# Optimization experiments

Measured on AMD Instinct MI355X. Metric: run time of the kernel, lower is better.

The kernel has to match this reference:

```python
import jax, jax.numpy as jnp
import numpy as np

N_ATOMS = 10000
N_HIDDEN = 75


def setup_inputs() -> dict:
    key = jax.random.key(0)
    k1, k2, k3, k4 = jax.random.split(key, 4)
    n_edges, n_pair_features = 64000, 14
    pair_features = jax.random.normal(k1, (n_edges, n_pair_features), dtype=jnp.float32)
    atom_features = jax.random.normal(k2, (N_ATOMS, N_HIDDEN), dtype=jnp.float32)
    atom_to_pair = jnp.sort(
        jax.random.randint(k3, (n_edges, 2), 0, N_ATOMS), axis=0
    ).astype(jnp.int64)
    # glorot_uniform for W [n_pair_features, n_hidden*n_hidden]
    fan_in, fan_out = n_pair_features, N_HIDDEN * N_HIDDEN
    limit = np.sqrt(6.0 / (fan_in + fan_out)).astype(np.float32)
    W = jax.random.uniform(k4, (fan_in, fan_out), minval=-limit, maxval=limit, dtype=jnp.float32)
    b = jnp.zeros((fan_out,), dtype=jnp.float32)
    return {"pair_features": pair_features, "atom_features": atom_features,
            "atom_to_pair": atom_to_pair, "W": W, "b": b}


def reference(pair_features, atom_features, atom_to_pair, W, b):
    # A: per-edge [n_hidden, n_hidden] matrices from pair features
    A = (pair_features @ W + b).reshape(-1, N_HIDDEN, N_HIDDEN)  # [E, H, H]
    # gather destination-atom features, batched matvec
    l = atom_features[atom_to_pair[:, 1]]                         # [E, H]
    out = jnp.einsum('ehk,ek->eh', A, l)                          # [E, H]
    # scatter-reduce to source atoms
    return jax.ops.segment_sum(out, atom_to_pair[:, 0], num_segments=N_ATOMS)
```

## Files before the change

kernel.cpp:

```cpp
#include <hip/hip_runtime.h>
#include <hip/hip_bf16.h>
#include <stdint.h>

constexpr int NA   = 10000;
constexpr int NH   = 75;
constexpr int NPF  = 14;
constexpr int NW   = 5625;
constexpr int NCOL = 1200;
constexpr int KP   = 104;
constexpr int MROW = 10112;
constexpr int WROW = 1208;
constexpr int JSL  = 38;

typedef __attribute__((ext_vector_type(8))) __bf16 bf16x8;
typedef __attribute__((ext_vector_type(4))) float floatx4;

__device__ __forceinline__ uint32_t f2bf_bits(float f) {
    uint32_t u = __float_as_uint(f);
    return (u + 0x7fffu + ((u >> 16) & 1u)) >> 16;
}
__device__ __forceinline__ float bf_lo(uint32_t w) { return __uint_as_float(w << 16); }
__device__ __forceinline__ float bf_hi(uint32_t w) { return __uint_as_float(w & 0xffff0000u); }

__device__ __forceinline__ void gload16(const void* g, void* l) {
    __builtin_amdgcn_global_load_lds(
        (const __attribute__((address_space(1))) uint32_t*)g,
        (__attribute__((address_space(3))) uint32_t*)l, 16, 0, 0);
}

__global__ __launch_bounds__(256) void k_prep(
    const float* __restrict__ af, const float* __restrict__ W,
    const float* __restrict__ bias, const int* __restrict__ atp,
    ushort* __restrict__ afb, ushort* __restrict__ wbt, int* __restrict__ rs,
    int E, int bA, int bW)
{
    const int b = blockIdx.x, tid = threadIdx.x;
    if (b < bA) {
        int idx = b * 256 + tid;
        if (idx >= MROW * (KP / 4)) return;
        int a = idx / (KP / 4), q = idx - a * (KP / 4);
        int k0 = q * 4;
        ushort4 st = {0, 0, 0, 0};
        if (a < NA) {
            float v[4];
            #pragma unroll
            for (int j = 0; j < 4; ++j) {
                int k = k0 + j;
                v[j] = (k < NH) ? af[a * NH + k] : 0.f;
            }
            st.x = (ushort)f2bf_bits(v[0]); st.y = (ushort)f2bf_bits(v[1]);
            st.z = (ushort)f2bf_bits(v[2]); st.w = (ushort)f2bf_bits(v[3]);
        }
        ((ushort4*)afb)[idx] = st;
    } else if (b < bA + bW) {
        int idx = (b - bA) * 256 + tid;
        if (idx >= WROW * (KP / 4)) return;
        int c = idx / (KP / 4), q = idx - c * (KP / 4);
        int k0 = q * 4;
        ushort4 st = {0, 0, 0, 0};
        if (c < NCOL) {
            int h = c >> 4, f = c & 15;
            float v[4] = {0.f, 0.f, 0.f, 0.f};
            #pragma unroll
            for (int j = 0; j < 4; ++j) {
                int k = k0 + j;
                if (k < NH) {
                    if (f < NPF)       v[j] = W[f * NW + h * NH + k];
                    else if (f == NPF) v[j] = bias[h * NH + k];
                }
            }
            st.x = (ushort)f2bf_bits(v[0]); st.y = (ushort)f2bf_bits(v[1]);
            st.z = (ushort)f2bf_bits(v[2]); st.w = (ushort)f2bf_bits(v[3]);
        }
        ((ushort4*)wbt)[idx] = st;
    } else {
        int e = (b - bA - bW) * 256 + tid;
        if (e >= E) return;
        int c  = atp[2 * e];
        int cp = (e == 0) ? -1 : atp[2 * (e - 1)];
        for (int a = cp + 1; a <= c; ++a) rs[a] = e;
        if (e == E - 1)
            for (int a = c + 1; a <= NA; ++a) rs[a] = E;
    }
}

__global__ __launch_bounds__(256) void k_gemm(const ushort* __restrict__ afb,
                                              const ushort* __restrict__ wbt,
                                              ushort* __restrict__ U) {
    __shared__ __align__(16) ushort sm[22016];
    ushort* As = sm;
    ushort* Bs = sm + 13312;

    const int tid  = threadIdx.x;
    const int lane = tid & 63, wid = tid >> 6;
    const int a0 = blockIdx.y * 128;
    const int c0 = blockIdx.x * 80;

    const char* aSrc = (const char*)(afb + (size_t)a0 * KP);
    const char* bSrc = (const char*)(wbt + (size_t)c0 * KP);

    for (int c = wid; c < 43; c += 4) {
        if (c < 26) gload16(aSrc + c * 1024 + lane * 16, (char*)As + c * 1024);
        else {
            int cb = c - 26;
            gload16(bSrc + cb * 1024 + lane * 16, (char*)Bs + cb * 1024);
        }
    }
    __syncthreads();

    const int lr = lane & 15;
    const int lk = (lane >> 4) * 8;
    floatx4 acc[5][2] = {};

    #pragma unroll
    for (int ks = 0; ks < 3; ++ks) {
        bf16x8 a[2], b[5];
        #pragma unroll
        for (int mf = 0; mf < 2; ++mf)
            a[mf] = *(const bf16x8*)&As[(wid * 32 + mf * 16 + lr) * KP + ks * 32 + lk];
        #pragma unroll
        for (int nf = 0; nf < 5; ++nf)
            b[nf] = *(const bf16x8*)&Bs[(nf * 16 + lr) * KP + ks * 32 + lk];
        #pragma unroll
        for (int nf = 0; nf < 5; ++nf)
            #pragma unroll
            for (int mf = 0; mf < 2; ++mf)
                acc[nf][mf] = __builtin_amdgcn_mfma_f32_16x16x32_bf16(
                    b[nf], a[mf], acc[nf][mf], 0, 0, 0);
    }

    #pragma unroll
    for (int mf = 0; mf < 2; ++mf) {
        int arow = a0 + wid * 32 + mf * 16 + lr;
        if (arow >= NA) continue;
        #pragma unroll
        for (int nf = 0; nf < 5; ++nf) {
            int cbase = c0 + nf * 16 + (lane >> 4) * 4;
            ushort4 st;
            st.x = (ushort)f2bf_bits(acc[nf][mf][0]);
            st.y = (ushort)f2bf_bits(acc[nf][mf][1]);
            st.z = (ushort)f2bf_bits(acc[nf][mf][2]);
            st.w = (ushort)f2bf_bits(acc[nf][mf][3]);
            *(ushort4*)&U[(size_t)arow * NCOL + cbase] = st;
        }
    }
}

__global__ __launch_bounds__(256) void k_edges2(
    const float* __restrict__ pf, const int* __restrict__ atp,
    const int* __restrict__ rs, const ushort* __restrict__ U,
    float* __restrict__ out)
{
    int idx = blockIdx.x * blockDim.x + threadIdx.x;
    if (idx >= NA * JSL) return;
    int a = idx / JSL;
    int j = idx - a * JSL;
    const bool two = (j + JSL) < NH;
    int e0 = rs[a], e1 = rs[a + 1];

    float acc0 = 0.f, acc1 = 0.f;
    for (int e = e0; e < e1; ++e) {
        int a1 = atp[2 * e + 1];
        const float* pfe = pf + (size_t)e * NPF;
        float p[14];
        #pragma unroll
        for (int f = 0; f < 7; ++f) {
            float2 t = *(const float2*)&pfe[2 * f];
            p[2 * f] = t.x; p[2 * f + 1] = t.y;
        }
        const ushort* ub = U + (size_t)a1 * NCOL;
        {
            const uint4* up = (const uint4*)(ub + j * 16);
            uint4 q0 = up[0], q1 = up[1];
            float s = bf_lo(q1.w);
            s += p[0]  * bf_lo(q0.x); s += p[1]  * bf_hi(q0.x);
            s += p[2]  * bf_lo(q0.y); s += p[3]  * bf_hi(q0.y);
            s += p[4]  * bf_lo(q0.z); s += p[5]  * bf_hi(q0.z);
            s += p[6]  * bf_lo(q0.w); s += p[7]  * bf_hi(q0.w);
            s += p[8]  * bf_lo(q1.x); s += p[9]  * bf_hi(q1.x);
            s += p[10] * bf_lo(q1.y); s += p[11] * bf_hi(q1.y);
            s += p[12] * bf_lo(q1.z); s += p[13] * bf_hi(q1.z);
            acc0 += s;
        }
        if (two) {
            const uint4* up = (const uint4*)(ub + (j + JSL) * 16);
            uint4 q0 = up[0], q1 = up[1];
            float s = bf_lo(q1.w);
            s += p[0]  * bf_lo(q0.x); s += p[1]  * bf_hi(q0.x);
            s += p[2]  * bf_lo(q0.y); s += p[3]  * bf_hi(q0.y);
            s += p[4]  * bf_lo(q0.z); s += p[5]  * bf_hi(q0.z);
            s += p[6]  * bf_lo(q0.w); s += p[7]  * bf_hi(q0.w);
            s += p[8]  * bf_lo(q1.x); s += p[9]  * bf_hi(q1.x);
            s += p[10] * bf_lo(q1.y); s += p[11] * bf_hi(q1.y);
            s += p[12] * bf_lo(q1.z); s += p[13] * bf_hi(q1.z);
            acc1 += s;
        }
    }
    out[a * NH + j] = acc0;
    if (two) out[a * NH + j + JSL] = acc1;
}

__global__ void k_naive(const float* __restrict__ pf, const float* __restrict__ af,
                        const int* __restrict__ atp, const float* __restrict__ W,
                        const float* __restrict__ bias, float* __restrict__ out, int E)
{
    int idx = blockIdx.x * blockDim.x + threadIdx.x;
    if (idx >= E * NH) return;
    int e = idx / NH, h = idx - e * NH;
    int a0 = atp[2 * e], a1 = atp[2 * e + 1];
    float p[NPF];
    #pragma unroll
    for (int f = 0; f < NPF; ++f) p[f] = pf[(size_t)e * NPF + f];
    float acc = 0.f;
    for (int k = 0; k < NH; ++k) {
        float w = bias[h * NH + k];
        #pragma unroll
        for (int f = 0; f < NPF; ++f) w += p[f] * W[f * NW + h * NH + k];
        acc += w * af[a1 * NH + k];
    }
    atomicAdd(&out[a0 * NH + h], acc);
}

extern "C" void kernel_launch(void* const* d_in, const int* in_sizes, int n_in,
                              void* d_out, int out_size, void* d_ws, size_t ws_size,
                              hipStream_t stream) {
    const float* pf   = (const float*)d_in[0];
    const float* af   = (const float*)d_in[1];
    const int*   atp  = (const int*)d_in[2];
    const float* W    = (const float*)d_in[3];
    const float* bias = (const float*)d_in[4];
    float* out = (float*)d_out;
    const int E = in_sizes[2] / 2;

    const size_t offAfb = 0;
    const size_t offWbt = offAfb + (size_t)MROW * KP * 2;
    const size_t offU   = offWbt + (size_t)WROW * KP * 2;
    const size_t offRs  = offU + (size_t)NA * NCOL * 2;
    const size_t need   = offRs + (size_t)(NA + 1) * sizeof(int);

    if (ws_size >= need) {
        ushort* afb = (ushort*)((char*)d_ws + offAfb);
        ushort* wbt = (ushort*)((char*)d_ws + offWbt);
        ushort* U   = (ushort*)((char*)d_ws + offU);
        int*    rs  = (int*)((char*)d_ws + offRs);

        const int bA = (MROW * (KP / 4) + 255) / 256;
        const int bW = (WROW * (KP / 4) + 255) / 256;
        const int bR = (E + 255) / 256;
        k_prep<<<bA + bW + bR, 256, 0, stream>>>(af, W, bias, atp, afb, wbt, rs, E, bA, bW);

        dim3 g1(NCOL / 80, MROW / 128);
        k_gemm<<<g1, 256, 0, stream>>>(afb, wbt, U);

        k_edges2<<<(NA * JSL + 255) / 256, 256, 0, stream>>>(pf, atp, rs, U, out);
    } else {
        hipMemsetAsync(d_out, 0, (size_t)out_size * sizeof(float), stream);
        k_naive<<<((size_t)E * NH + 255) / 256, 256, 0, stream>>>(pf, af, atp, W, bias, out, E);
    }
}
```

Measured before the change: 41.48 us.

## Switch intermediates to fp16 with packed dot2 edge reduction and wider GEMM tile

Converts the atom-feature, weight and intermediate U buffers from bf16 to fp16, and uses fp16 MFMA plus a packed round-toward-zero conversion for the GEMM output. A new prep stage packs the pair features to fp16 with a trailing 1.0 for the bias slot, so the edge kernel can do each 16-term dot product in eight fdot2 instructions instead of sixteen scalar FMAs with bf16 unpacking. The GEMM N tile grows from 80 to 240 columns, which enlarges LDS use and the accumulator register count. In exchange, fp16 has less range than bf16 and adds an extra pair-feature buffer write and read.

```diff
diff --git a/kernel.cpp b/kernel.cpp
--- a/kernel.cpp
+++ b/kernel.cpp
@@ -11,16 +11,21 @@
 constexpr int MROW = 10112;
 constexpr int WROW = 1208;
 constexpr int JSL  = 38;
-
-typedef __attribute__((ext_vector_type(8))) __bf16 bf16x8;
+constexpr int BN   = 240;
+constexpr int ACH  = 26;
+constexpr int BCH  = 49;
+
+typedef _Float16 f16;
+typedef __attribute__((ext_vector_type(2))) _Float16 f16x2;
+typedef __attribute__((ext_vector_type(8))) _Float16 f16x8;
 typedef __attribute__((ext_vector_type(4))) float floatx4;
 
-__device__ __forceinline__ uint32_t f2bf_bits(float f) {
-    uint32_t u = __float_as_uint(f);
-    return (u + 0x7fffu + ((u >> 16) & 1u)) >> 16;
-}
-__device__ __forceinline__ float bf_lo(uint32_t w) { return __uint_as_float(w << 16); }
-__device__ __forceinline__ float bf_hi(uint32_t w) { return __uint_as_float(w & 0xffff0000u); }
+__device__ __forceinline__ ushort f2h_bits(float f) {
+    return __builtin_bit_cast(ushort, (f16)f);
+}
+__device__ __forceinline__ f16x2 bch(uint32_t w) {
+    return __builtin_bit_cast(f16x2, w);
+}
 
 __device__ __forceinline__ void gload16(const void* g, void* l) {
     __builtin_amdgcn_global_load_lds(
@@ -28,11 +33,25 @@
         (__attribute__((address_space(3))) uint32_t*)l, 16, 0, 0);
 }
 
+__device__ __forceinline__ float dot16(uint4 p0, uint4 p1, uint4 u0, uint4 u1, float c) {
+    c = __builtin_amdgcn_fdot2(bch(p0.x), bch(u0.x), c, false);
+    c = __builtin_amdgcn_fdot2(bch(p0.y), bch(u0.y), c, false);
+    c = __builtin_amdgcn_fdot2(bch(p0.z), bch(u0.z), c, false);
+    c = __builtin_amdgcn_fdot2(bch(p0.w), bch(u0.w), c, false);
+    c = __builtin_amdgcn_fdot2(bch(p1.x), bch(u1.x), c, false);
+    c = __builtin_amdgcn_fdot2(bch(p1.y), bch(u1.y), c, false);
+    c = __builtin_amdgcn_fdot2(bch(p1.z), bch(u1.z), c, false);
+    c = __builtin_amdgcn_fdot2(bch(p1.w), bch(u1.w), c, false);
+    return c;
+}
+
 __global__ __launch_bounds__(256) void k_prep(
     const float* __restrict__ af, const float* __restrict__ W,
-    const float* __restrict__ bias, const int* __restrict__ atp,
-    ushort* __restrict__ afb, ushort* __restrict__ wbt, int* __restrict__ rs,
-    int E, int bA, int bW)
+    const float* __restrict__ bias, const float* __restrict__ pf,
+    const int* __restrict__ atp,
+    ushort* __restrict__ afb, ushort* __restrict__ wbt,
+    ushort* __restrict__ pfh, int* __restrict__ rs,
+    int E, int bA, int bW, int bP)
 {
     const int b = blockIdx.x, tid = threadIdx.x;
     if (b < bA) {
@@ -48,8 +67,8 @@
                 int k = k0 + j;
                 v[j] = (k < NH) ? af[a * NH + k] : 0.f;
             }
-            st.x = (ushort)f2bf_bits(v[0]); st.y = (ushort)f2bf_bits(v[1]);
-            st.z = (ushort)f2bf_bits(v[2]); st.w = (ushort)f2bf_bits(v[3]);
+            st.x = f2h_bits(v[0]); st.y = f2h_bits(v[1]);
+            st.z = f2h_bits(v[2]); st.w = f2h_bits(v[3]);
         }
         ((ushort4*)afb)[idx] = st;
     } else if (b < bA + bW) {
@@ -69,12 +88,27 @@
                     else if (f == NPF) v[j] = bias[h * NH + k];
                 }
             }
-            st.x = (ushort)f2bf_bits(v[0]); st.y = (ushort)f2bf_bits(v[1]);
-            st.z = (ushort)f2bf_bits(v[2]); st.w = (ushort)f2bf_bits(v[3]);
+            st.x = f2h_bits(v[0]); st.y = f2h_bits(v[1]);
+            st.z = f2h_bits(v[2]); st.w = f2h_bits(v[3]);
         }
         ((ushort4*)wbt)[idx] = st;
+    } else if (b < bA + bW + bP) {
+        int e = (b - bA - bW) * 256 + tid;
+        if (e >= E) return;
+        const float* pfe = pf + (size_t)e * NPF;
+        union { f16 h[16]; uint4 q[2]; } u;
+        #pragma unroll
+        for (int f = 0; f < 7; ++f) {
+            float2 t = *(const float2*)&pfe[2 * f];
+            u.h[2 * f]     = (f16)t.x;
+            u.h[2 * f + 1] = (f16)t.y;
+        }
+        u.h[14] = (f16)1.0f;
+        u.h[15] = (f16)0.0f;
+        uint4* dst = (uint4*)(pfh + (size_t)e * 16);
+        dst[0] = u.q[0]; dst[1] = u.q[1];
     } else {
-        int e = (b - bA - bW) * 256 + tid;
+        int e = (b - bA - bW - bP) * 256 + tid;
         if (e >= E) return;
         int c  = atp[2 * e];
         int cp = (e == 0) ? -1 : atp[2 * (e - 1)];
@@ -84,25 +118,25 @@
     }
 }
 
-__global__ __launch_bounds__(256) void k_gemm(const ushort* __restrict__ afb,
-                                              const ushort* __restrict__ wbt,
-                                              ushort* __restrict__ U) {
-    __shared__ __align__(16) ushort sm[22016];
+__global__ __launch_bounds__(256, 2) void k_gemm(const ushort* __restrict__ afb,
+                                                 const ushort* __restrict__ wbt,
+                                                 ushort* __restrict__ U) {
+    __shared__ __align__(16) ushort sm[38400];
     ushort* As = sm;
     ushort* Bs = sm + 13312;
 
     const int tid  = threadIdx.x;
     const int lane = tid & 63, wid = tid >> 6;
     const int a0 = blockIdx.y * 128;
-    const int c0 = blockIdx.x * 80;
+    const int c0 = blockIdx.x * BN;
 
     const char* aSrc = (const char*)(afb + (size_t)a0 * KP);
     const char* bSrc = (const char*)(wbt + (size_t)c0 * KP);
 
-    for (int c = wid; c < 43; c += 4) {
-        if (c < 26) gload16(aSrc + c * 1024 + lane * 16, (char*)As + c * 1024);
+    for (int c = wid; c < ACH + BCH; c += 4) {
+        if (c < ACH) gload16(aSrc + c * 1024 + lane * 16, (char*)As + c * 1024);
         else {
-            int cb = c - 26;
+            int cb = c - ACH;
             gload16(bSrc + cb * 1024 + lane * 16, (char*)Bs + cb * 1024);
         }
     }
@@ -110,23 +144,23 @@
 
     const int lr = lane & 15;
     const int lk = (lane >> 4) * 8;
-    floatx4 acc[5][2] = {};
+    floatx4 acc[15][2] = {};
 
     #pragma unroll
     for (int ks = 0; ks < 3; ++ks) {
-        bf16x8 a[2], b[5];
+        f16x8 a[2], bv[15];
         #pragma unroll
         for (int mf = 0; mf < 2; ++mf)
-            a[mf] = *(const bf16x8*)&As[(wid * 32 + mf * 16 + lr) * KP + ks * 32 + lk];
-        #pragma unroll
-        for (int nf = 0; nf < 5; ++nf)
-            b[nf] = *(const bf16x8*)&Bs[(nf * 16 + lr) * KP + ks * 32 + lk];
-        #pragma unroll
-        for (int nf = 0; nf < 5; ++nf)
+            a[mf] = *(const f16x8*)&As[(wid * 32 + mf * 16 + lr) * KP + ks * 32 + lk];
+        #pragma unroll
+        for (int nf = 0; nf < 15; ++nf)
+            bv[nf] = *(const f16x8*)&Bs[(nf * 16 + lr) * KP + ks * 32 + lk];
+        #pragma unroll
+        for (int nf = 0; nf < 15; ++nf)
             #pragma unroll
             for (int mf = 0; mf < 2; ++mf)
-                acc[nf][mf] = __builtin_amdgcn_mfma_f32_16x16x32_bf16(
-                    b[nf], a[mf], acc[nf][mf], 0, 0, 0);
+                acc[nf][mf] = __builtin_amdgcn_mfma_f32_16x16x32_f16(
+                    bv[nf], a[mf], acc[nf][mf], 0, 0, 0);
     }
 
     #pragma unroll
@@ -134,20 +168,20 @@
         int arow = a0 + wid * 32 + mf * 16 + lr;
         if (arow >= NA) continue;
         #pragma unroll
-        for (int nf = 0; nf < 5; ++nf) {
+        for (int nf = 0; nf < 15; ++nf) {
             int cbase = c0 + nf * 16 + (lane >> 4) * 4;
-            ushort4 st;
-            st.x = (ushort)f2bf_bits(acc[nf][mf][0]);
-            st.y = (ushort)f2bf_bits(acc[nf][mf][1]);
-            st.z = (ushort)f2bf_bits(acc[nf][mf][2]);
-            st.w = (ushort)f2bf_bits(acc[nf][mf][3]);
-            *(ushort4*)&U[(size_t)arow * NCOL + cbase] = st;
+            uint2 st;
+            st.x = __builtin_bit_cast(uint32_t,
+                     __builtin_amdgcn_cvt_pkrtz(acc[nf][mf][0], acc[nf][mf][1]));
+            st.y = __builtin_bit_cast(uint32_t,
+                     __builtin_amdgcn_cvt_pkrtz(acc[nf][mf][2], acc[nf][mf][3]));
+            *(uint2*)&U[(size_t)arow * NCOL + cbase] = st;
         }
     }
 }
 
 __global__ __launch_bounds__(256) void k_edges2(
-    const float* __restrict__ pf, const int* __restrict__ atp,
+    const ushort* __restrict__ pfh, const int* __restrict__ atp,
     const int* __restrict__ rs, const ushort* __restrict__ U,
     float* __restrict__ out)
 {
@@ -161,39 +195,16 @@
     float acc0 = 0.f, acc1 = 0.f;
     for (int e = e0; e < e1; ++e) {
         int a1 = atp[2 * e + 1];
-        const float* pfe = pf + (size_t)e * NPF;
-        float p[14];
-        #pragma unroll
-        for (int f = 0; f < 7; ++f) {
-            float2 t = *(const float2*)&pfe[2 * f];
-            p[2 * f] = t.x; p[2 * f + 1] = t.y;
-        }
+        const uint4* pq = (const uint4*)(pfh + (size_t)e * 16);
+        uint4 p0 = pq[0], p1 = pq[1];
         const ushort* ub = U + (size_t)a1 * NCOL;
         {
             const uint4* up = (const uint4*)(ub + j * 16);
-            uint4 q0 = up[0], q1 = up[1];
-            float s = bf_lo(q1.w);
-            s += p[0]  * bf_lo(q0.x); s += p[1]  * bf_hi(q0.x);
-            s += p[2]  * bf_lo(q0.y); s += p[3]  * bf_hi(q0.y);
-            s += p[4]  * bf_lo(q0.z); s += p[5]  * bf_hi(q0.z);
-            s += p[6]  * bf_lo(q0.w); s += p[7]  * bf_hi(q0.w);
-            s += p[8]  * bf_lo(q1.x); s += p[9]  * bf_hi(q1.x);
-            s += p[10] * bf_lo(q1.y); s += p[11] * bf_hi(q1.y);
-            s += p[12] * bf_lo(q1.z); s += p[13] * bf_hi(q1.z);
-            acc0 += s;
+            acc0 = dot16(p0, p1, up[0], up[1], acc0);
         }
         if (two) {
             const uint4* up = (const uint4*)(ub + (j + JSL) * 16);
-            uint4 q0 = up[0], q1 = up[1];
-            float s = bf_lo(q1.w);
-            s += p[0]  * bf_lo(q0.x); s += p[1]  * bf_hi(q0.x);
-            s += p[2]  * bf_lo(q0.y); s += p[3]  * bf_hi(q0.y);
-            s += p[4]  * bf_lo(q0.z); s += p[5]  * bf_hi(q0.z);
-            s += p[6]  * bf_lo(q0.w); s += p[7]  * bf_hi(q0.w);
-            s += p[8]  * bf_lo(q1.x); s += p[9]  * bf_hi(q1.x);
-            s += p[10] * bf_lo(q1.y); s += p[11] * bf_hi(q1.y);
-            s += p[12] * bf_lo(q1.z); s += p[13] * bf_hi(q1.z);
-            acc1 += s;
+            acc1 = dot16(p0, p1, up[0], up[1], acc1);
         }
     }
     out[a * NH + j] = acc0;
@@ -235,24 +246,28 @@
     const size_t offAfb = 0;
     const size_t offWbt = offAfb + (size_t)MROW * KP * 2;
     const size_t offU   = offWbt + (size_t)WROW * KP * 2;
-    const size_t offRs  = offU + (size_t)NA * NCOL * 2;
+    const size_t offPfh = offU + (size_t)NA * NCOL * 2;
+    const size_t offRs  = offPfh + (size_t)E * 16 * 2;
     const size_t need   = offRs + (size_t)(NA + 1) * sizeof(int);
 
     if (ws_size >= need) {
         ushort* afb = (ushort*)((char*)d_ws + offAfb);
         ushort* wbt = (ushort*)((char*)d_ws + offWbt);
         ushort* U   = (ushort*)((char*)d_ws + offU);
+        ushort* pfh = (ushort*)((char*)d_ws + offPfh);
         int*    rs  = (int*)((char*)d_ws + offRs);
 
         const int bA = (MROW * (KP / 4) + 255) / 256;
         const int bW = (WROW * (KP / 4) + 255) / 256;
+        const int bP = (E + 255) / 256;
         const int bR = (E + 255) / 256;
-        k_prep<<<bA + bW + bR, 256, 0, stream>>>(af, W, bias, atp, afb, wbt, rs, E, bA, bW);
-
-        dim3 g1(NCOL / 80, MROW / 128);
+        k_prep<<<bA + bW + bP + bR, 256, 0, stream>>>(af, W, bias, pf, atp,
+                                                      afb, wbt, pfh, rs, E, bA, bW, bP);
+
+        dim3 g1(NCOL / BN, MROW / 128);
         k_gemm<<<g1, 256, 0, stream>>>(afb, wbt, U);
 
-        k_edges2<<<(NA * JSL + 255) / 256, 256, 0, stream>>>(pf, atp, rs, U, out);
+        k_edges2<<<(NA * JSL + 255) / 256, 256, 0, stream>>>(pfh, atp, rs, U, out);
     } else {
         hipMemsetAsync(d_out, 0, (size_t)out_size * sizeof(float), stream);
         k_naive<<<((size_t)E * NH + 255) / 256, 256, 0, stream>>>(pf, af, atp, W, bias, out, E);
```

Result: faster. 37.67 us (-9.2%).
